# Kernel tuning notes

Measured on AMD Instinct MI355X. Metric: run time of the kernel, lower is better.

Reference implementation:

```python
import jax, jax.numpy as jnp
import numpy as np

N_NODES = 100000
N_EDGES = 800000
N_ETYPES = 5
NUM_GRAPHS = 64
IN_DIM, HID_DIM, OUT_DIM = 23, 128, 64


def setup_inputs() -> dict:
    key = jax.random.key(0)
    ks = jax.random.split(key, 8)
    x = jax.random.normal(ks[0], (N_NODES, IN_DIM), dtype=jnp.float32)
    edges = jax.random.randint(ks[1], (N_ETYPES, 2, N_EDGES), 0, N_NODES, dtype=jnp.int32)
    graph_ids = jnp.sort(jax.random.randint(ks[2], (N_NODES,), 0, NUM_GRAPHS, dtype=jnp.int32))
    # Per-edge-type SAGEConv(gcn) params: fc_neigh weight + bias, two layers.
    W1 = jax.random.normal(ks[3], (N_ETYPES, IN_DIM, HID_DIM), dtype=jnp.float32) / np.sqrt(IN_DIM)
    b1 = jnp.zeros((N_ETYPES, HID_DIM), dtype=jnp.float32)
    W2 = jax.random.normal(ks[4], (N_ETYPES, HID_DIM, OUT_DIM), dtype=jnp.float32) / np.sqrt(HID_DIM)
    b2 = jnp.zeros((N_ETYPES, OUT_DIM), dtype=jnp.float32)
    return {"x": x, "edges": edges, "graph_ids": graph_ids,
            "W1": W1, "b1": b1, "W2": W2, "b2": b2}


def _hetero_sage_gcn(h, edges, W, b):
    """HeteroGraphConv(sum) of SAGEConv(aggregator='gcn') over edge types.
    h: [N, d_in]; edges: [T, 2, E]; W: [T, d_in, d_out]; b: [T, d_out]."""
    n = h.shape[0]

    def per_etype(e, We, be):
        src, dst = e[0], e[1]                                   # [E]
        deg = jax.ops.segment_sum(jnp.ones_like(dst, h.dtype), dst, num_segments=n)
        neigh = jax.ops.segment_sum(h[src], dst, num_segments=n)  # [N, d_in]
        h_neigh = (neigh + h) / (deg[:, None] + 1.0)              # gcn: include self
        return h_neigh @ We + be                                  # fc_neigh only

    outs = jax.vmap(per_etype)(edges, W, b)  # [T, N, d_out]
    return outs.sum(0)


def reference(x, edges, graph_ids, W1, b1, W2, b2):
    h = jax.nn.relu(_hetero_sage_gcn(x, edges, W1, b1))  # dropout = identity (eval)
    h = _hetero_sage_gcn(h, edges, W2, b2)
    counts = jax.ops.segment_sum(jnp.ones(h.shape[0], h.dtype), graph_ids,
                                 num_segments=NUM_GRAPHS)
    pooled = jax.ops.segment_sum(h, graph_ids, num_segments=NUM_GRAPHS)
    return pooled / jnp.maximum(counts, 1.0)[:, None]  # dgl.mean_nodes -> [G, out]
```

## Files before the change

kernel.cpp:

```cpp
#include <hip/hip_runtime.h>

#define N_NODES 100000
#define N_EDGES 800000
#define N_ETYPES 5
#define NUM_GRAPHS 64
#define IN_DIM 23
#define HID_DIM 128
#define OUT_DIM 64
#define N_KEYS (N_NODES * N_ETYPES)
#define KPB 2048
#define NBINS ((N_KEYS + KPB - 1) / KPB)
#define BIN_CAP 18432
#define CHUNK 8192
#define TOT_EDGES (N_EDGES * N_ETYPES)

typedef unsigned short u16;
typedef unsigned int u32;
using short8 = __attribute__((ext_vector_type(8))) short;
using f32x4  = __attribute__((ext_vector_type(4))) float;

__device__ __forceinline__ float bf2f(u16 v) {
    union { unsigned u; float f; } x; x.u = ((unsigned)v) << 16; return x.f;
}
__device__ __forceinline__ float lo2f(u32 v) {
    union { unsigned u; float f; } x; x.u = v << 16; return x.f;
}
__device__ __forceinline__ float hi2f(u32 v) {
    union { unsigned u; float f; } x; x.u = v & 0xffff0000u; return x.f;
}
__device__ __forceinline__ u16 f2bf(float f) {
    union { float f; unsigned u; } x; x.f = f;
    unsigned r = x.u + 0x7fff + ((x.u >> 16) & 1);
    return (u16)(r >> 16);
}

__global__ __launch_bounds__(256) void k_prep(const float* __restrict__ W1,
                                              const float* __restrict__ W2,
                                              const float* __restrict__ b1,
                                              u16* __restrict__ w1t,
                                              u16* __restrict__ w2t,
                                              float* __restrict__ b1s) {
    int stride = gridDim.x * 256;
    int g0 = blockIdx.x * 256 + threadIdx.x;
    for (int i = g0; i < HID_DIM * 160; i += stride) {
        int hid = i / 160, k = i - hid * 160;
        int t = k >> 5, f = k & 31;
        w1t[i] = (f < IN_DIM) ? f2bf(W1[((size_t)t * IN_DIM + f) * HID_DIM + hid]) : (u16)0;
    }
    for (int i = g0; i < N_ETYPES * OUT_DIM * HID_DIM; i += stride) {
        int t = i >> 13, r = i & 8191;
        int out = r >> 7, k = r & 127;
        w2t[i] = f2bf(W2[((size_t)t * HID_DIM + k) * OUT_DIM + out]);
    }
    for (int i = g0; i < HID_DIM; i += stride) {
        float s = 0.f;
        #pragma unroll
        for (int t = 0; t < N_ETYPES; ++t) s += b1[t * HID_DIM + i];
        b1s[i] = s;
    }
}

__global__ __launch_bounds__(256) void k_xb(const float* __restrict__ x,
                                            u16* __restrict__ xb) {
    int i = blockIdx.x * 256 + threadIdx.x;
    if (i >= N_NODES * 32) return;
    int n = i >> 5, f = i & 31;
    xb[i] = (f < IN_DIM) ? f2bf(x[(size_t)n * IN_DIM + f]) : (u16)0;
}

__global__ __launch_bounds__(256) void k_bin(const int* __restrict__ edges,
                                             int* __restrict__ bin_cnt,
                                             int* __restrict__ binned) {
    __shared__ int s_key[CHUNK];
    __shared__ int s_hist[4][256];
    __shared__ int s_base[4][256];
    int tid = threadIdx.x;
    int w = tid >> 6;
    int g0 = blockIdx.x * CHUNK;
    int nch = TOT_EDGES - g0; if (nch > CHUNK) nch = CHUNK;
    for (int i = tid; i < 4 * 256; i += 256) ((int*)s_hist)[i] = 0;
    __syncthreads();
    for (int i = tid; i < nch; i += 256) {
        int gi = g0 + i;
        int t = (unsigned)gi / (unsigned)N_EDGES;
        int e = gi - t * N_EDGES;
        int dst = edges[((size_t)t * 2 + 1) * N_EDGES + e];
        int key = dst * N_ETYPES + t;
        s_key[i] = key;
        atomicAdd(&s_hist[w][key >> 11], 1);
    }
    __syncthreads();
    for (int i = tid; i < NBINS; i += 256) {
        int h0 = s_hist[0][i], h1 = s_hist[1][i], h2 = s_hist[2][i], h3 = s_hist[3][i];
        int h = h0 + h1 + h2 + h3;
        int base = h ? atomicAdd(&bin_cnt[i], h) : 0;
        s_base[0][i] = base;
        s_base[1][i] = base + h0;
        s_base[2][i] = base + h0 + h1;
        s_base[3][i] = base + h0 + h1 + h2;
    }
    __syncthreads();
    for (int i = tid; i < nch; i += 256) {
        int gi = g0 + i;
        int t = (unsigned)gi / (unsigned)N_EDGES;
        int e = gi - t * N_EDGES;
        int src = edges[((size_t)t * 2 + 0) * N_EDGES + e];
        int key = s_key[i];
        int bin = key >> 11;
        int pos = atomicAdd(&s_base[w][bin], 1);
        if (pos < BIN_CAP)
            binned[(size_t)bin * BIN_CAP + pos] = ((key & 2047) << 17) | src;
    }
}

__global__ __launch_bounds__(256) void k_csr(const int* __restrict__ bin_cnt,
                                             const int* __restrict__ binned,
                                             int* __restrict__ rowptr,
                                             int* __restrict__ csr) {
    __shared__ int s_cnt[KPB];
    __shared__ int s_ofs[KPB];
    __shared__ int s_red[256];
    int tid = threadIdx.x;
    int b = blockIdx.x;
    int ps = 0;
    for (int i = tid; i < b; i += 256) ps += bin_cnt[i];
    s_red[tid] = ps;
    __syncthreads();
    for (int s = 128; s > 0; s >>= 1) {
        if (tid < s) s_red[tid] += s_red[tid + s];
        __syncthreads();
    }
    int csr_base = s_red[0];
    __syncthreads();
    int cnt_b = bin_cnt[b];
    if (cnt_b > BIN_CAP) cnt_b = BIN_CAP;
    int key0 = b * KPB;
    int keys_in = N_KEYS - key0; if (keys_in > KPB) keys_in = KPB;
    for (int i = tid; i < KPB; i += 256) s_cnt[i] = 0;
    __syncthreads();
    const int* ep = binned + (size_t)b * BIN_CAP;
    for (int i = tid; i < cnt_b; i += 256)
        atomicAdd(&s_cnt[ep[i] >> 17], 1);
    __syncthreads();
    int loc[8]; int base_t = 0;
    #pragma unroll
    for (int q = 0; q < 8; ++q) { loc[q] = base_t; base_t += s_cnt[tid * 8 + q]; }
    s_red[tid] = base_t;
    __syncthreads();
    for (int s = 1; s < 256; s <<= 1) {
        int add = (tid >= s) ? s_red[tid - s] : 0;
        __syncthreads();
        s_red[tid] += add;
        __syncthreads();
    }
    int excl = (tid == 0) ? 0 : s_red[tid - 1];
    #pragma unroll
    for (int q = 0; q < 8; ++q) {
        int k = tid * 8 + q;
        int o = excl + loc[q];
        s_ofs[k] = o;
        if (k < keys_in) rowptr[key0 + k] = csr_base + o;
    }
    if (b == NBINS - 1 && tid == 0) rowptr[N_KEYS] = csr_base + cnt_b;
    __syncthreads();
    for (int i = tid; i < cnt_b; i += 256) {
        int entry = ep[i];
        int pos = atomicAdd(&s_ofs[entry >> 17], 1);
        csr[csr_base + pos] = entry & 0x1FFFF;
    }
}

__global__ __launch_bounds__(256) void k_gather1(const int* __restrict__ rowptr,
                                                 const int* __restrict__ csr,
                                                 const u32* __restrict__ xb32,
                                                 u32* __restrict__ acat32) {
    int tid = threadIdx.x;
    int lane = tid & 15;
    int lanebase = tid & 48;
    int n = blockIdx.x * 16 + (tid >> 4);
    int t = blockIdx.y;
    int key = n * N_ETYPES + t;
    int rp0 = rowptr[key];
    int deg = rowptr[key + 1] - rp0;
    int stage = csr[rp0 + lane];
    int kmax = deg < 16 ? deg : 16;
    u32 v = xb32[(size_t)n * 16 + lane];
    float acc0 = lo2f(v), acc1 = hi2f(v);
    float a00 = 0.f, a01 = 0.f, a10 = 0.f, a11 = 0.f;
    int k = 0;
    for (; k + 1 < kmax; k += 2) {
        int s0 = __shfl(stage, lanebase + k);
        int s1 = __shfl(stage, lanebase + k + 1);
        u32 v0 = xb32[(size_t)s0 * 16 + lane];
        u32 v1 = xb32[(size_t)s1 * 16 + lane];
        a00 += lo2f(v0); a01 += hi2f(v0);
        a10 += lo2f(v1); a11 += hi2f(v1);
    }
    if (k < kmax) {
        int s0 = __shfl(stage, lanebase + k);
        u32 v0 = xb32[(size_t)s0 * 16 + lane];
        a00 += lo2f(v0); a01 += hi2f(v0);
        ++k;
    }
    for (; k < deg; ++k) {
        int s0 = csr[rp0 + k];
        u32 v0 = xb32[(size_t)s0 * 16 + lane];
        a00 += lo2f(v0); a01 += hi2f(v0);
    }
    acc0 += a00 + a10;
    acc1 += a01 + a11;
    float inv = 1.0f / (float)(deg + 1);
    if (lane < 12)
        acat32[(size_t)n * 60 + t * 12 + lane] =
            (u32)f2bf(acc0 * inv) | ((u32)f2bf(acc1 * inv) << 16);
}

__global__ __launch_bounds__(256) void k_gemm12(const u16* __restrict__ acat,
                                                const u16* __restrict__ w1t,
                                                const u16* __restrict__ w2t,
                                                const float* __restrict__ b1s,
                                                u16* __restrict__ g,
                                                int gt0, int gt1) {
    __shared__ u16 s_a[64 * 168];
    __shared__ u16 s_h1[64 * 136];
    u16* s_out = s_a;
    int tid = threadIdx.x;
    int base = blockIdx.x * 64;

    for (int i = tid; i < 64 * 40; i += 256) {
        int r = i / 40, col4 = i - r * 40;
        int t = col4 >> 3, q4 = col4 & 7;
        ushort4 v = {0, 0, 0, 0};
        if (q4 < 6 && base + r < N_NODES)
            v = *(const ushort4*)&acat[(size_t)(base + r) * 120 + t * 24 + q4 * 4];
        *(ushort4*)&s_a[r * 168 + t * 32 + q4 * 4] = v;
    }
    __syncthreads();

    int l = tid & 63, w = tid >> 6;
    int lr = l & 15, lg = l >> 4;

    short8 a5[5];
    #pragma unroll
    for (int ks = 0; ks < 5; ++ks)
        a5[ks] = *(const short8*)&s_a[(w * 16 + lr) * 168 + ks * 32 + lg * 8];
    {
        f32x4 acc[8];
        #pragma unroll
        for (int nt = 0; nt < 8; ++nt) acc[nt] = (f32x4){0.f, 0.f, 0.f, 0.f};
        #pragma unroll
        for (int nt = 0; nt < 8; ++nt) {
            #pragma unroll
            for (int ks = 0; ks < 5; ++ks) {
                short8 b = *(const short8*)&w1t[(nt * 16 + lr) * 160 + ks * 32 + lg * 8];
                acc[nt] = __builtin_amdgcn_mfma_f32_16x16x32_bf16(a5[ks], b, acc[nt], 0, 0, 0);
            }
        }
        #pragma unroll
        for (int nt = 0; nt < 8; ++nt) {
            float bias = b1s[nt * 16 + lr];
            #pragma unroll
            for (int r = 0; r < 4; ++r) {
                float h = acc[nt][r] + bias;
                s_h1[(w * 16 + lg * 4 + r) * 136 + nt * 16 + lr] = f2bf(h > 0.f ? h : 0.f);
            }
        }
    }
    __syncthreads();

    short8 a2[4];
    #pragma unroll
    for (int ks = 0; ks < 4; ++ks)
        a2[ks] = *(const short8*)&s_h1[(w * 16 + lr) * 136 + ks * 32 + lg * 8];
    for (int t = gt0; t < gt1; ++t) {
        f32x4 acc2[4];
        #pragma unroll
        for (int nt = 0; nt < 4; ++nt) acc2[nt] = (f32x4){0.f, 0.f, 0.f, 0.f};
        #pragma unroll
        for (int nt = 0; nt < 4; ++nt) {
            #pragma unroll
            for (int ks = 0; ks < 4; ++ks) {
                short8 b = *(const short8*)&w2t[((size_t)t * OUT_DIM + nt * 16 + lr) * HID_DIM + ks * 32 + lg * 8];
                acc2[nt] = __builtin_amdgcn_mfma_f32_16x16x32_bf16(a2[ks], b, acc2[nt], 0, 0, 0);
            }
        }
        __syncthreads();
        #pragma unroll
        for (int nt = 0; nt < 4; ++nt)
            #pragma unroll
            for (int r = 0; r < 4; ++r)
                s_out[(w * 16 + lg * 4 + r) * 72 + nt * 16 + lr] = f2bf(acc2[nt][r]);
        __syncthreads();
        size_t pb = (size_t)(t - gt0) * N_NODES;
        #pragma unroll
        for (int j = 0; j < 4; ++j) {
            int flat = j * 256 + tid;
            int rrow = flat >> 4, c4 = (flat & 15) * 4;
            int n = base + rrow;
            if (n < N_NODES)
                *(ushort4*)&g[(pb + n) * OUT_DIM + c4] = *(const ushort4*)&s_out[rrow * 72 + c4];
        }
    }
}

__global__ __launch_bounds__(256) void k_gather2(const int* __restrict__ rowptr,
                                                 const int* __restrict__ csr,
                                                 const u32* __restrict__ g32,
                                                 u32* __restrict__ h232) {
    int tid = threadIdx.x;
    int lane = tid & 31;
    int lanebase = tid & 32;
    int n = blockIdx.x * 8 + (tid >> 5);
    int kb = n * N_ETYPES;
    float acc0 = 0.f, acc1 = 0.f;
    for (int tc = 0; tc < N_ETYPES; ++tc) {
        int rp0 = rowptr[kb + tc];
        int deg = rowptr[kb + tc + 1] - rp0;
        int stage = csr[rp0 + lane];
        int kmax = deg < 32 ? deg : 32;
        const u32* gp = g32 + (size_t)tc * N_NODES * 32;
        u32 v = gp[(size_t)n * 32 + lane];
        float s0 = lo2f(v), s1 = hi2f(v), s2 = 0.f, s3 = 0.f;
        int k = 0;
        for (; k + 1 < kmax; k += 2) {
            int p0 = __shfl(stage, lanebase + k);
            int p1 = __shfl(stage, lanebase + k + 1);
            u32 v0 = gp[(size_t)p0 * 32 + lane];
            u32 v1 = gp[(size_t)p1 * 32 + lane];
            s0 += lo2f(v0); s1 += hi2f(v0);
            s2 += lo2f(v1); s3 += hi2f(v1);
        }
        if (k < kmax) {
            int p0 = __shfl(stage, lanebase + k);
            u32 v0 = gp[(size_t)p0 * 32 + lane];
            s0 += lo2f(v0); s1 += hi2f(v0);
            ++k;
        }
        for (; k < deg; ++k) {
            int p0 = csr[rp0 + k];
            u32 v0 = gp[(size_t)p0 * 32 + lane];
            s0 += lo2f(v0); s1 += hi2f(v0);
        }
        float inv = 1.0f / (float)(deg + 1);
        acc0 += (s0 + s2) * inv;
        acc1 += (s1 + s3) * inv;
    }
    h232[(size_t)n * 32 + lane] = (u32)f2bf(acc0) | ((u32)f2bf(acc1) << 16);
}

__global__ __launch_bounds__(256) void k_pool1(const u16* __restrict__ h2,
                                               const int* __restrict__ gids,
                                               float* __restrict__ out_acc) {
    int w = threadIdx.x >> 6, lane = threadIdx.x & 63;
    int n0 = blockIdx.x * 256 + w * 64;
    int nend = n0 + 64; if (nend > N_NODES) nend = N_NODES;
    float acc = 0.f;
    int cur = -1;
    for (int n = n0; n < nend; ++n) {
        int gid = gids[n];
        if (gid != cur) {
            if (cur >= 0) atomicAdd(&out_acc[cur * OUT_DIM + lane], acc);
            acc = 0.f; cur = gid;
        }
        acc += bf2f(h2[(size_t)n * OUT_DIM + lane]);
    }
    if (cur >= 0) atomicAdd(&out_acc[cur * OUT_DIM + lane], acc);
}

__global__ __launch_bounds__(64) void k_pool2(const float* __restrict__ out_acc,
                                              const int* __restrict__ gids,
                                              const float* __restrict__ b2,
                                              float* __restrict__ out) {
    int gid = blockIdx.x, j = threadIdx.x;
    int lo = 0, hi = N_NODES;
    while (lo < hi) { int mid = (lo + hi) >> 1; if (gids[mid] < gid) lo = mid + 1; else hi = mid; }
    int start = lo;
    hi = N_NODES;
    while (lo < hi) { int mid = (lo + hi) >> 1; if (gids[mid] < gid + 1) lo = mid + 1; else hi = mid; }
    int count = lo - start;
    float b = 0.f;
    #pragma unroll
    for (int t = 0; t < N_ETYPES; ++t) b += b2[t * OUT_DIM + j];
    float c = (float)count;
    out[gid * OUT_DIM + j] = (out_acc[gid * OUT_DIM + j] + c * b) / fmaxf(c, 1.0f);
}

extern "C" void kernel_launch(void* const* d_in, const int* in_sizes, int n_in,
                              void* d_out, int out_size, void* d_ws, size_t ws_size,
                              hipStream_t stream) {
    const float* x    = (const float*)d_in[0];
    const int*   edges= (const int*)d_in[1];
    const int*   gids = (const int*)d_in[2];
    const float* W1   = (const float*)d_in[3];
    const float* b1   = (const float*)d_in[4];
    const float* W2   = (const float*)d_in[5];
    const float* b2   = (const float*)d_in[6];
    float* out = (float*)d_out;

    int*   bin_cnt = (int*)d_ws;
    int*   rowptr  = bin_cnt + 256;
    int*   csr     = bin_cnt + 500272;
    u16*   xb      = (u16*)(bin_cnt + 4500352);
    u16*   w1t     = (u16*)(bin_cnt + 6100352);
    u16*   w2t     = (u16*)(bin_cnt + 6110592);
    float* b1s     = (float*)(bin_cnt + 6131072);
    u16*   acat    = (u16*)(bin_cnt + 6131200);
    u16*   g       = (u16*)(bin_cnt + 12131200);
    int*   binned  = bin_cnt + 12131200;
    u16*   h2      = (u16*)(bin_cnt + 28131200);
    float* out_acc = (float*)(bin_cnt + 31331200);

    hipMemsetAsync(bin_cnt, 0, 256 * sizeof(int), stream);
    hipMemsetAsync(out_acc, 0, NUM_GRAPHS * OUT_DIM * sizeof(float), stream);

    k_prep<<<80, 256, 0, stream>>>(W1, W2, b1, w1t, w2t, b1s);
    k_xb<<<(N_NODES * 32 + 255) / 256, 256, 0, stream>>>(x, xb);
    k_bin<<<(TOT_EDGES + CHUNK - 1) / CHUNK, 256, 0, stream>>>(edges, bin_cnt, binned);
    k_csr<<<NBINS, 256, 0, stream>>>(bin_cnt, binned, rowptr, csr);

    k_gather1<<<dim3(N_NODES / 16, N_ETYPES), 256, 0, stream>>>(
        rowptr, csr, (const u32*)xb, (u32*)acat);

    int nblk = (N_NODES + 63) / 64;
    k_gemm12<<<nblk, 256, 0, stream>>>(acat, w1t, w2t, b1s, g, 0, 5);
    k_gather2<<<N_NODES / 8, 256, 0, stream>>>(rowptr, csr, (const u32*)g, (u32*)h2);

    k_pool1<<<(N_NODES + 255) / 256, 256, 0, stream>>>(h2, gids, out_acc);
    k_pool2<<<NUM_GRAPHS, 64, 0, stream>>>(out_acc, gids, b2, out);
}
```

Measured before the change: 420.6 us.

## Split neighbor gathers across lane groups with shuffle reductions; fuse x conversion into prep

Both gather kernels now give each node a larger lane group split into four sub-groups. Each sub-group walks every fourth neighbor and loads two words per lane, and the partial sums are combined with xor shuffles. This puts more neighbor loads in flight per node to hide latency on the random-access gather, at the cost of more threads per node and extra shuffle reductions. Separately, the bf16 conversion of x is folded into k_prep as a grid-stride loop, removing one kernel launch, and k_prep's grid grows to 1024 blocks.

```diff
diff --git a/kernel.cpp b/kernel.cpp
--- a/kernel.cpp
+++ b/kernel.cpp
@@ -37,9 +37,11 @@
 __global__ __launch_bounds__(256) void k_prep(const float* __restrict__ W1,
                                               const float* __restrict__ W2,
                                               const float* __restrict__ b1,
+                                              const float* __restrict__ x,
                                               u16* __restrict__ w1t,
                                               u16* __restrict__ w2t,
-                                              float* __restrict__ b1s) {
+                                              float* __restrict__ b1s,
+                                              u16* __restrict__ xb) {
     int stride = gridDim.x * 256;
     int g0 = blockIdx.x * 256 + threadIdx.x;
     for (int i = g0; i < HID_DIM * 160; i += stride) {
@@ -58,14 +60,10 @@
         for (int t = 0; t < N_ETYPES; ++t) s += b1[t * HID_DIM + i];
         b1s[i] = s;
     }
-}
-
-__global__ __launch_bounds__(256) void k_xb(const float* __restrict__ x,
-                                            u16* __restrict__ xb) {
-    int i = blockIdx.x * 256 + threadIdx.x;
-    if (i >= N_NODES * 32) return;
-    int n = i >> 5, f = i & 31;
-    xb[i] = (f < IN_DIM) ? f2bf(x[(size_t)n * IN_DIM + f]) : (u16)0;
+    for (int i = g0; i < N_NODES * 32; i += stride) {
+        int n = i >> 5, f = i & 31;
+        xb[i] = (f < IN_DIM) ? f2bf(x[(size_t)n * IN_DIM + f]) : (u16)0;
+    }
 }
 
 __global__ __launch_bounds__(256) void k_bin(const int* __restrict__ edges,
@@ -175,44 +173,68 @@
                                                  const u32* __restrict__ xb32,
                                                  u32* __restrict__ acat32) {
     int tid = threadIdx.x;
-    int lane = tid & 15;
-    int lanebase = tid & 48;
-    int n = blockIdx.x * 16 + (tid >> 4);
+    int lane = tid & 31;
+    int fl = lane & 7;
+    int sub = lane >> 3;
+    int lanebase = tid & 32;
+    int n = blockIdx.x * 8 + (tid >> 5);
     int t = blockIdx.y;
     int key = n * N_ETYPES + t;
     int rp0 = rowptr[key];
     int deg = rowptr[key + 1] - rp0;
     int stage = csr[rp0 + lane];
-    int kmax = deg < 16 ? deg : 16;
-    u32 v = xb32[(size_t)n * 16 + lane];
-    float acc0 = lo2f(v), acc1 = hi2f(v);
-    float a00 = 0.f, a01 = 0.f, a10 = 0.f, a11 = 0.f;
-    int k = 0;
-    for (; k + 1 < kmax; k += 2) {
-        int s0 = __shfl(stage, lanebase + k);
-        int s1 = __shfl(stage, lanebase + k + 1);
-        u32 v0 = xb32[(size_t)s0 * 16 + lane];
-        u32 v1 = xb32[(size_t)s1 * 16 + lane];
-        a00 += lo2f(v0); a01 += hi2f(v0);
-        a10 += lo2f(v1); a11 += hi2f(v1);
-    }
-    if (k < kmax) {
-        int s0 = __shfl(stage, lanebase + k);
-        u32 v0 = xb32[(size_t)s0 * 16 + lane];
-        a00 += lo2f(v0); a01 += hi2f(v0);
-        ++k;
-    }
-    for (; k < deg; ++k) {
-        int s0 = csr[rp0 + k];
-        u32 v0 = xb32[(size_t)s0 * 16 + lane];
-        a00 += lo2f(v0); a01 += hi2f(v0);
-    }
-    acc0 += a00 + a10;
-    acc1 += a01 + a11;
-    float inv = 1.0f / (float)(deg + 1);
-    if (lane < 12)
-        acat32[(size_t)n * 60 + t * 12 + lane] =
-            (u32)f2bf(acc0 * inv) | ((u32)f2bf(acc1 * inv) << 16);
+    int kmax = deg < 32 ? deg : 32;
+    int kend = (kmax + 3) & ~3;
+    float a0 = 0.f, a1 = 0.f, a2 = 0.f, a3 = 0.f;
+    if (sub == 0) {
+        u32 v0 = xb32[(size_t)n * 16 + fl * 2];
+        u32 v1 = xb32[(size_t)n * 16 + fl * 2 + 1];
+        a0 = lo2f(v0); a1 = hi2f(v0); a2 = lo2f(v1); a3 = hi2f(v1);
+    }
+    int k = sub;
+    for (; k + 4 < kend; k += 8) {
+        int sA = __shfl(stage, lanebase + k);
+        int sB = __shfl(stage, lanebase + k + 4);
+        if (k < kmax) {
+            u32 vA0 = xb32[(size_t)sA * 16 + fl * 2];
+            u32 vA1 = xb32[(size_t)sA * 16 + fl * 2 + 1];
+            a0 += lo2f(vA0); a1 += hi2f(vA0);
+            a2 += lo2f(vA1); a3 += hi2f(vA1);
+        }
+        if (k + 4 < kmax) {
+            u32 vB0 = xb32[(size_t)sB * 16 + fl * 2];
+            u32 vB1 = xb32[(size_t)sB * 16 + fl * 2 + 1];
+            a0 += lo2f(vB0); a1 += hi2f(vB0);
+            a2 += lo2f(vB1); a3 += hi2f(vB1);
+        }
+    }
+    if (k < kend) {
+        int sA = __shfl(stage, lanebase + k);
+        if (k < kmax) {
+            u32 vA0 = xb32[(size_t)sA * 16 + fl * 2];
+            u32 vA1 = xb32[(size_t)sA * 16 + fl * 2 + 1];
+            a0 += lo2f(vA0); a1 += hi2f(vA0);
+            a2 += lo2f(vA1); a3 += hi2f(vA1);
+        }
+    }
+    for (int kk = 32 + sub; kk < deg; kk += 4) {
+        int sA = csr[rp0 + kk];
+        u32 vA0 = xb32[(size_t)sA * 16 + fl * 2];
+        u32 vA1 = xb32[(size_t)sA * 16 + fl * 2 + 1];
+        a0 += lo2f(vA0); a1 += hi2f(vA0);
+        a2 += lo2f(vA1); a3 += hi2f(vA1);
+    }
+    a0 += __shfl_xor(a0, 8);  a1 += __shfl_xor(a1, 8);
+    a2 += __shfl_xor(a2, 8);  a3 += __shfl_xor(a3, 8);
+    a0 += __shfl_xor(a0, 16); a1 += __shfl_xor(a1, 16);
+    a2 += __shfl_xor(a2, 16); a3 += __shfl_xor(a3, 16);
+    if (sub == 0 && fl < 6) {
+        float inv = 1.0f / (float)(deg + 1);
+        uint2 o;
+        o.x = (u32)f2bf(a0 * inv) | ((u32)f2bf(a1 * inv) << 16);
+        o.y = (u32)f2bf(a2 * inv) | ((u32)f2bf(a3 * inv) << 16);
+        *(uint2*)&acat32[(size_t)n * 60 + t * 12 + fl * 2] = o;
+    }
 }
 
 __global__ __launch_bounds__(256) void k_gemm12(const u16* __restrict__ acat,
@@ -308,44 +330,72 @@
                                                  const u32* __restrict__ g32,
                                                  u32* __restrict__ h232) {
     int tid = threadIdx.x;
-    int lane = tid & 31;
-    int lanebase = tid & 32;
-    int n = blockIdx.x * 8 + (tid >> 5);
+    int lane = tid & 63;
+    int fl = lane & 15;
+    int sub = lane >> 4;
+    int n = blockIdx.x * 4 + (tid >> 6);
     int kb = n * N_ETYPES;
-    float acc0 = 0.f, acc1 = 0.f;
+    float acc0 = 0.f, acc1 = 0.f, acc2 = 0.f, acc3 = 0.f;
     for (int tc = 0; tc < N_ETYPES; ++tc) {
         int rp0 = rowptr[kb + tc];
         int deg = rowptr[kb + tc + 1] - rp0;
         int stage = csr[rp0 + lane];
-        int kmax = deg < 32 ? deg : 32;
+        int kmax = deg < 64 ? deg : 64;
+        int kend = (kmax + 3) & ~3;
         const u32* gp = g32 + (size_t)tc * N_NODES * 32;
-        u32 v = gp[(size_t)n * 32 + lane];
-        float s0 = lo2f(v), s1 = hi2f(v), s2 = 0.f, s3 = 0.f;
-        int k = 0;
-        for (; k + 1 < kmax; k += 2) {
-            int p0 = __shfl(stage, lanebase + k);
-            int p1 = __shfl(stage, lanebase + k + 1);
-            u32 v0 = gp[(size_t)p0 * 32 + lane];
-            u32 v1 = gp[(size_t)p1 * 32 + lane];
-            s0 += lo2f(v0); s1 += hi2f(v0);
-            s2 += lo2f(v1); s3 += hi2f(v1);
-        }
-        if (k < kmax) {
-            int p0 = __shfl(stage, lanebase + k);
-            u32 v0 = gp[(size_t)p0 * 32 + lane];
-            s0 += lo2f(v0); s1 += hi2f(v0);
-            ++k;
-        }
-        for (; k < deg; ++k) {
-            int p0 = csr[rp0 + k];
-            u32 v0 = gp[(size_t)p0 * 32 + lane];
-            s0 += lo2f(v0); s1 += hi2f(v0);
+        float s0 = 0.f, s1 = 0.f, s2 = 0.f, s3 = 0.f;
+        if (sub == 0) {
+            u32 v0 = gp[(size_t)n * 32 + fl * 2];
+            u32 v1 = gp[(size_t)n * 32 + fl * 2 + 1];
+            s0 = lo2f(v0); s1 = hi2f(v0); s2 = lo2f(v1); s3 = hi2f(v1);
+        }
+        int k = sub;
+        for (; k + 4 < kend; k += 8) {
+            int pA = __shfl(stage, k);
+            int pB = __shfl(stage, k + 4);
+            if (k < kmax) {
+                u32 vA0 = gp[(size_t)pA * 32 + fl * 2];
+                u32 vA1 = gp[(size_t)pA * 32 + fl * 2 + 1];
+                s0 += lo2f(vA0); s1 += hi2f(vA0);
+                s2 += lo2f(vA1); s3 += hi2f(vA1);
+            }
+            if (k + 4 < kmax) {
+                u32 vB0 = gp[(size_t)pB * 32 + fl * 2];
+                u32 vB1 = gp[(size_t)pB * 32 + fl * 2 + 1];
+                s0 += lo2f(vB0); s1 += hi2f(vB0);
+                s2 += lo2f(vB1); s3 += hi2f(vB1);
+            }
+        }
+        if (k < kend) {
+            int pA = __shfl(stage, k);
+            if (k < kmax) {
+                u32 vA0 = gp[(size_t)pA * 32 + fl * 2];
+                u32 vA1 = gp[(size_t)pA * 32 + fl * 2 + 1];
+                s0 += lo2f(vA0); s1 += hi2f(vA0);
+                s2 += lo2f(vA1); s3 += hi2f(vA1);
+            }
+        }
+        for (int kk = 64 + sub; kk < deg; kk += 4) {
+            int pA = csr[rp0 + kk];
+            u32 vA0 = gp[(size_t)pA * 32 + fl * 2];
+            u32 vA1 = gp[(size_t)pA * 32 + fl * 2 + 1];
+            s0 += lo2f(vA0); s1 += hi2f(vA0);
+            s2 += lo2f(vA1); s3 += hi2f(vA1);
         }
         float inv = 1.0f / (float)(deg + 1);
-        acc0 += (s0 + s2) * inv;
-        acc1 += (s1 + s3) * inv;
-    }
-    h232[(size_t)n * 32 + lane] = (u32)f2bf(acc0) | ((u32)f2bf(acc1) << 16);
+        acc0 += s0 * inv; acc1 += s1 * inv;
+        acc2 += s2 * inv; acc3 += s3 * inv;
+    }
+    acc0 += __shfl_xor(acc0, 16); acc1 += __shfl_xor(acc1, 16);
+    acc2 += __shfl_xor(acc2, 16); acc3 += __shfl_xor(acc3, 16);
+    acc0 += __shfl_xor(acc0, 32); acc1 += __shfl_xor(acc1, 32);
+    acc2 += __shfl_xor(acc2, 32); acc3 += __shfl_xor(acc3, 32);
+    if (sub == 0) {
+        uint2 o;
+        o.x = (u32)f2bf(acc0) | ((u32)f2bf(acc1) << 16);
+        o.y = (u32)f2bf(acc2) | ((u32)f2bf(acc3) << 16);
+        *(uint2*)&h232[(size_t)n * 32 + fl * 2] = o;
+    }
 }
 
 __global__ __launch_bounds__(256) void k_pool1(const u16* __restrict__ h2,
@@ -413,17 +463,16 @@
     hipMemsetAsync(bin_cnt, 0, 256 * sizeof(int), stream);
     hipMemsetAsync(out_acc, 0, NUM_GRAPHS * OUT_DIM * sizeof(float), stream);
 
-    k_prep<<<80, 256, 0, stream>>>(W1, W2, b1, w1t, w2t, b1s);
-    k_xb<<<(N_NODES * 32 + 255) / 256, 256, 0, stream>>>(x, xb);
+    k_prep<<<1024, 256, 0, stream>>>(W1, W2, b1, x, w1t, w2t, b1s, xb);
     k_bin<<<(TOT_EDGES + CHUNK - 1) / CHUNK, 256, 0, stream>>>(edges, bin_cnt, binned);
     k_csr<<<NBINS, 256, 0, stream>>>(bin_cnt, binned, rowptr, csr);
 
-    k_gather1<<<dim3(N_NODES / 16, N_ETYPES), 256, 0, stream>>>(
+    k_gather1<<<dim3(N_NODES / 8, N_ETYPES), 256, 0, stream>>>(
         rowptr, csr, (const u32*)xb, (u32*)acat);
 
     int nblk = (N_NODES + 63) / 64;
     k_gemm12<<<nblk, 256, 0, stream>>>(acat, w1t, w2t, b1s, g, 0, 5);
-    k_gather2<<<N_NODES / 8, 256, 0, stream>>>(rowptr, csr, (const u32*)g, (u32*)h2);
+    k_gather2<<<N_NODES / 4, 256, 0, stream>>>(rowptr, csr, (const u32*)g, (u32*)h2);
 
     k_pool1<<<(N_NODES + 255) / 256, 256, 0, stream>>>(h2, gids, out_acc);
     k_pool2<<<NUM_GRAPHS, 64, 0, stream>>>(out_acc, gids, b2, out);
```

After: 452.0 us. 1.07x slower.

## Fuse prep kernels into binning launch and widen gather loads to 8 bytes

Applied to the files above, without the earlier changes.

Folds the weight/bias prep and x-to-bf16 conversion into extra blocks of the binning kernel, removing two launches and letting that conversion run alongside binning. Both gather kernels now use half as many lanes per node, each loading uint2 (four bf16 values) per neighbor, with 4-way unrolled neighbor loops and the index stage split across two registers. This is meant to raise bytes per memory request and memory-level parallelism in the latency-bound gathers. In exchange it adds register pressure, and the k_bin prep blocks now have to cover the whole of xb with only 64 blocks.

```diff
diff --git a/kernel.cpp b/kernel.cpp
--- a/kernel.cpp
+++ b/kernel.cpp
@@ -13,6 +13,8 @@
 #define BIN_CAP 18432
 #define CHUNK 8192
 #define TOT_EDGES (N_EDGES * N_ETYPES)
+#define BIN_BLOCKS ((TOT_EDGES + CHUNK - 1) / CHUNK)
+#define PREP_BLOCKS 64
 
 typedef unsigned short u16;
 typedef unsigned int u32;
@@ -34,47 +36,48 @@
     return (u16)(r >> 16);
 }
 
-__global__ __launch_bounds__(256) void k_prep(const float* __restrict__ W1,
-                                              const float* __restrict__ W2,
-                                              const float* __restrict__ b1,
-                                              u16* __restrict__ w1t,
-                                              u16* __restrict__ w2t,
-                                              float* __restrict__ b1s) {
-    int stride = gridDim.x * 256;
-    int g0 = blockIdx.x * 256 + threadIdx.x;
-    for (int i = g0; i < HID_DIM * 160; i += stride) {
-        int hid = i / 160, k = i - hid * 160;
-        int t = k >> 5, f = k & 31;
-        w1t[i] = (f < IN_DIM) ? f2bf(W1[((size_t)t * IN_DIM + f) * HID_DIM + hid]) : (u16)0;
-    }
-    for (int i = g0; i < N_ETYPES * OUT_DIM * HID_DIM; i += stride) {
-        int t = i >> 13, r = i & 8191;
-        int out = r >> 7, k = r & 127;
-        w2t[i] = f2bf(W2[((size_t)t * HID_DIM + k) * OUT_DIM + out]);
-    }
-    for (int i = g0; i < HID_DIM; i += stride) {
-        float s = 0.f;
-        #pragma unroll
-        for (int t = 0; t < N_ETYPES; ++t) s += b1[t * HID_DIM + i];
-        b1s[i] = s;
-    }
-}
-
-__global__ __launch_bounds__(256) void k_xb(const float* __restrict__ x,
-                                            u16* __restrict__ xb) {
-    int i = blockIdx.x * 256 + threadIdx.x;
-    if (i >= N_NODES * 32) return;
-    int n = i >> 5, f = i & 31;
-    xb[i] = (f < IN_DIM) ? f2bf(x[(size_t)n * IN_DIM + f]) : (u16)0;
-}
-
 __global__ __launch_bounds__(256) void k_bin(const int* __restrict__ edges,
                                              int* __restrict__ bin_cnt,
-                                             int* __restrict__ binned) {
+                                             int* __restrict__ binned,
+                                             const float* __restrict__ W1,
+                                             const float* __restrict__ W2,
+                                             const float* __restrict__ b1,
+                                             const float* __restrict__ x,
+                                             u16* __restrict__ w1t,
+                                             u16* __restrict__ w2t,
+                                             float* __restrict__ b1s,
+                                             u16* __restrict__ xb) {
     __shared__ int s_key[CHUNK];
     __shared__ int s_hist[4][256];
     __shared__ int s_base[4][256];
     int tid = threadIdx.x;
+
+    if (blockIdx.x >= BIN_BLOCKS) {
+        int stride = PREP_BLOCKS * 256;
+        int g0 = (blockIdx.x - BIN_BLOCKS) * 256 + tid;
+        for (int i = g0; i < HID_DIM * 160; i += stride) {
+            int hid = i / 160, k = i - hid * 160;
+            int t = k >> 5, f = k & 31;
+            w1t[i] = (f < IN_DIM) ? f2bf(W1[((size_t)t * IN_DIM + f) * HID_DIM + hid]) : (u16)0;
+        }
+        for (int i = g0; i < N_ETYPES * OUT_DIM * HID_DIM; i += stride) {
+            int t = i >> 13, r = i & 8191;
+            int out = r >> 7, k = r & 127;
+            w2t[i] = f2bf(W2[((size_t)t * HID_DIM + k) * OUT_DIM + out]);
+        }
+        for (int i = g0; i < HID_DIM; i += stride) {
+            float s = 0.f;
+            #pragma unroll
+            for (int t = 0; t < N_ETYPES; ++t) s += b1[t * HID_DIM + i];
+            b1s[i] = s;
+        }
+        for (int i = g0; i < N_NODES * 32; i += stride) {
+            int n = i >> 5, f = i & 31;
+            xb[i] = (f < IN_DIM) ? f2bf(x[(size_t)n * IN_DIM + f]) : (u16)0;
+        }
+        return;
+    }
+
     int w = tid >> 6;
     int g0 = blockIdx.x * CHUNK;
     int nch = TOT_EDGES - g0; if (nch > CHUNK) nch = CHUNK;
@@ -175,44 +178,72 @@
                                                  const u32* __restrict__ xb32,
                                                  u32* __restrict__ acat32) {
     int tid = threadIdx.x;
-    int lane = tid & 15;
-    int lanebase = tid & 48;
-    int n = blockIdx.x * 16 + (tid >> 4);
+    int fl = tid & 7;
+    int lanebase = tid & 56;
+    int n = blockIdx.x * 32 + (tid >> 3);
     int t = blockIdx.y;
     int key = n * N_ETYPES + t;
     int rp0 = rowptr[key];
     int deg = rowptr[key + 1] - rp0;
-    int stage = csr[rp0 + lane];
+    int stageA = csr[rp0 + fl];
+    int stageB = csr[rp0 + 8 + fl];
     int kmax = deg < 16 ? deg : 16;
-    u32 v = xb32[(size_t)n * 16 + lane];
-    float acc0 = lo2f(v), acc1 = hi2f(v);
-    float a00 = 0.f, a01 = 0.f, a10 = 0.f, a11 = 0.f;
+    int kA = kmax < 8 ? kmax : 8;
+    uint2 v = *(const uint2*)&xb32[(size_t)n * 16 + fl * 2];
+    float a0 = lo2f(v.x), a1 = hi2f(v.x), a2 = lo2f(v.y), a3 = hi2f(v.y);
+    float b0 = 0.f, b1v = 0.f, b2 = 0.f, b3 = 0.f;
     int k = 0;
-    for (; k + 1 < kmax; k += 2) {
-        int s0 = __shfl(stage, lanebase + k);
-        int s1 = __shfl(stage, lanebase + k + 1);
-        u32 v0 = xb32[(size_t)s0 * 16 + lane];
-        u32 v1 = xb32[(size_t)s1 * 16 + lane];
-        a00 += lo2f(v0); a01 += hi2f(v0);
-        a10 += lo2f(v1); a11 += hi2f(v1);
-    }
-    if (k < kmax) {
-        int s0 = __shfl(stage, lanebase + k);
-        u32 v0 = xb32[(size_t)s0 * 16 + lane];
-        a00 += lo2f(v0); a01 += hi2f(v0);
-        ++k;
-    }
-    for (; k < deg; ++k) {
+    for (; k + 3 < kA; k += 4) {
+        int s0 = __shfl(stageA, lanebase + k);
+        int s1 = __shfl(stageA, lanebase + k + 1);
+        int s2 = __shfl(stageA, lanebase + k + 2);
+        int s3 = __shfl(stageA, lanebase + k + 3);
+        uint2 v0 = *(const uint2*)&xb32[(size_t)s0 * 16 + fl * 2];
+        uint2 v1 = *(const uint2*)&xb32[(size_t)s1 * 16 + fl * 2];
+        uint2 v2 = *(const uint2*)&xb32[(size_t)s2 * 16 + fl * 2];
+        uint2 v3 = *(const uint2*)&xb32[(size_t)s3 * 16 + fl * 2];
+        a0 += lo2f(v0.x); a1 += hi2f(v0.x); a2 += lo2f(v0.y); a3 += hi2f(v0.y);
+        b0 += lo2f(v1.x); b1v += hi2f(v1.x); b2 += lo2f(v1.y); b3 += hi2f(v1.y);
+        a0 += lo2f(v2.x); a1 += hi2f(v2.x); a2 += lo2f(v2.y); a3 += hi2f(v2.y);
+        b0 += lo2f(v3.x); b1v += hi2f(v3.x); b2 += lo2f(v3.y); b3 += hi2f(v3.y);
+    }
+    for (; k < kA; ++k) {
+        int s0 = __shfl(stageA, lanebase + k);
+        uint2 v0 = *(const uint2*)&xb32[(size_t)s0 * 16 + fl * 2];
+        a0 += lo2f(v0.x); a1 += hi2f(v0.x); a2 += lo2f(v0.y); a3 += hi2f(v0.y);
+    }
+    for (k = 8; k + 3 < kmax; k += 4) {
+        int s0 = __shfl(stageB, lanebase + k - 8);
+        int s1 = __shfl(stageB, lanebase + k - 7);
+        int s2 = __shfl(stageB, lanebase + k - 6);
+        int s3 = __shfl(stageB, lanebase + k - 5);
+        uint2 v0 = *(const uint2*)&xb32[(size_t)s0 * 16 + fl * 2];
+        uint2 v1 = *(const uint2*)&xb32[(size_t)s1 * 16 + fl * 2];
+        uint2 v2 = *(const uint2*)&xb32[(size_t)s2 * 16 + fl * 2];
+        uint2 v3 = *(const uint2*)&xb32[(size_t)s3 * 16 + fl * 2];
+        a0 += lo2f(v0.x); a1 += hi2f(v0.x); a2 += lo2f(v0.y); a3 += hi2f(v0.y);
+        b0 += lo2f(v1.x); b1v += hi2f(v1.x); b2 += lo2f(v1.y); b3 += hi2f(v1.y);
+        a0 += lo2f(v2.x); a1 += hi2f(v2.x); a2 += lo2f(v2.y); a3 += hi2f(v2.y);
+        b0 += lo2f(v3.x); b1v += hi2f(v3.x); b2 += lo2f(v3.y); b3 += hi2f(v3.y);
+    }
+    for (; k < kmax && k >= 8; ++k) {
+        int s0 = __shfl(stageB, lanebase + k - 8);
+        uint2 v0 = *(const uint2*)&xb32[(size_t)s0 * 16 + fl * 2];
+        a0 += lo2f(v0.x); a1 += hi2f(v0.x); a2 += lo2f(v0.y); a3 += hi2f(v0.y);
+    }
+    for (k = 16; k < deg; ++k) {
         int s0 = csr[rp0 + k];
-        u32 v0 = xb32[(size_t)s0 * 16 + lane];
-        a00 += lo2f(v0); a01 += hi2f(v0);
-    }
-    acc0 += a00 + a10;
-    acc1 += a01 + a11;
-    float inv = 1.0f / (float)(deg + 1);
-    if (lane < 12)
-        acat32[(size_t)n * 60 + t * 12 + lane] =
-            (u32)f2bf(acc0 * inv) | ((u32)f2bf(acc1 * inv) << 16);
+        uint2 v0 = *(const uint2*)&xb32[(size_t)s0 * 16 + fl * 2];
+        a0 += lo2f(v0.x); a1 += hi2f(v0.x); a2 += lo2f(v0.y); a3 += hi2f(v0.y);
+    }
+    a0 += b0; a1 += b1v; a2 += b2; a3 += b3;
+    if (fl < 6) {
+        float inv = 1.0f / (float)(deg + 1);
+        uint2 o;
+        o.x = (u32)f2bf(a0 * inv) | ((u32)f2bf(a1 * inv) << 16);
+        o.y = (u32)f2bf(a2 * inv) | ((u32)f2bf(a3 * inv) << 16);
+        *(uint2*)&acat32[(size_t)n * 60 + t * 12 + fl * 2] = o;
+    }
 }
 
 __global__ __launch_bounds__(256) void k_gemm12(const u16* __restrict__ acat,
@@ -308,44 +339,76 @@
                                                  const u32* __restrict__ g32,
                                                  u32* __restrict__ h232) {
     int tid = threadIdx.x;
-    int lane = tid & 31;
-    int lanebase = tid & 32;
-    int n = blockIdx.x * 8 + (tid >> 5);
+    int fl = tid & 15;
+    int lanebase = tid & 48;
+    int n = blockIdx.x * 16 + (tid >> 4);
     int kb = n * N_ETYPES;
-    float acc0 = 0.f, acc1 = 0.f;
+    float acc0 = 0.f, acc1 = 0.f, acc2 = 0.f, acc3 = 0.f;
     for (int tc = 0; tc < N_ETYPES; ++tc) {
         int rp0 = rowptr[kb + tc];
         int deg = rowptr[kb + tc + 1] - rp0;
-        int stage = csr[rp0 + lane];
+        int stageA = csr[rp0 + fl];
+        int stageB = csr[rp0 + 16 + fl];
         int kmax = deg < 32 ? deg : 32;
+        int kA = kmax < 16 ? kmax : 16;
         const u32* gp = g32 + (size_t)tc * N_NODES * 32;
-        u32 v = gp[(size_t)n * 32 + lane];
-        float s0 = lo2f(v), s1 = hi2f(v), s2 = 0.f, s3 = 0.f;
+        uint2 v = *(const uint2*)&gp[(size_t)n * 32 + fl * 2];
+        float s0 = lo2f(v.x), s1 = hi2f(v.x), s2 = lo2f(v.y), s3 = hi2f(v.y);
+        float r0 = 0.f, r1 = 0.f, r2 = 0.f, r3 = 0.f;
         int k = 0;
-        for (; k + 1 < kmax; k += 2) {
-            int p0 = __shfl(stage, lanebase + k);
-            int p1 = __shfl(stage, lanebase + k + 1);
-            u32 v0 = gp[(size_t)p0 * 32 + lane];
-            u32 v1 = gp[(size_t)p1 * 32 + lane];
-            s0 += lo2f(v0); s1 += hi2f(v0);
-            s2 += lo2f(v1); s3 += hi2f(v1);
-        }
-        if (k < kmax) {
-            int p0 = __shfl(stage, lanebase + k);
-            u32 v0 = gp[(size_t)p0 * 32 + lane];
-            s0 += lo2f(v0); s1 += hi2f(v0);
-            ++k;
-        }
-        for (; k < deg; ++k) {
+        for (; k + 3 < kA; k += 4) {
+            int p0 = __shfl(stageA, lanebase + k);
+            int p1 = __shfl(stageA, lanebase + k + 1);
+            int p2 = __shfl(stageA, lanebase + k + 2);
+            int p3 = __shfl(stageA, lanebase + k + 3);
+            uint2 v0 = *(const uint2*)&gp[(size_t)p0 * 32 + fl * 2];
+            uint2 v1 = *(const uint2*)&gp[(size_t)p1 * 32 + fl * 2];
+            uint2 v2 = *(const uint2*)&gp[(size_t)p2 * 32 + fl * 2];
+            uint2 v3 = *(const uint2*)&gp[(size_t)p3 * 32 + fl * 2];
+            s0 += lo2f(v0.x); s1 += hi2f(v0.x); s2 += lo2f(v0.y); s3 += hi2f(v0.y);
+            r0 += lo2f(v1.x); r1 += hi2f(v1.x); r2 += lo2f(v1.y); r3 += hi2f(v1.y);
+            s0 += lo2f(v2.x); s1 += hi2f(v2.x); s2 += lo2f(v2.y); s3 += hi2f(v2.y);
+            r0 += lo2f(v3.x); r1 += hi2f(v3.x); r2 += lo2f(v3.y); r3 += hi2f(v3.y);
+        }
+        for (; k < kA; ++k) {
+            int p0 = __shfl(stageA, lanebase + k);
+            uint2 v0 = *(const uint2*)&gp[(size_t)p0 * 32 + fl * 2];
+            s0 += lo2f(v0.x); s1 += hi2f(v0.x); s2 += lo2f(v0.y); s3 += hi2f(v0.y);
+        }
+        for (k = 16; k + 3 < kmax; k += 4) {
+            int p0 = __shfl(stageB, lanebase + k - 16);
+            int p1 = __shfl(stageB, lanebase + k - 15);
+            int p2 = __shfl(stageB, lanebase + k - 14);
+            int p3 = __shfl(stageB, lanebase + k - 13);
+            uint2 v0 = *(const uint2*)&gp[(size_t)p0 * 32 + fl * 2];
+            uint2 v1 = *(const uint2*)&gp[(size_t)p1 * 32 + fl * 2];
+            uint2 v2 = *(const uint2*)&gp[(size_t)p2 * 32 + fl * 2];
+            uint2 v3 = *(const uint2*)&gp[(size_t)p3 * 32 + fl * 2];
+            s0 += lo2f(v0.x); s1 += hi2f(v0.x); s2 += lo2f(v0.y); s3 += hi2f(v0.y);
+            r0 += lo2f(v1.x); r1 += hi2f(v1.x); r2 += lo2f(v1.y); r3 += hi2f(v1.y);
+            s0 += lo2f(v2.x); s1 += hi2f(v2.x); s2 += lo2f(v2.y); s3 += hi2f(v2.y);
+            r0 += lo2f(v3.x); r1 += hi2f(v3.x); r2 += lo2f(v3.y); r3 += hi2f(v3.y);
+        }
+        for (; k < kmax && k >= 16; ++k) {
+            int p0 = __shfl(stageB, lanebase + k - 16);
+            uint2 v0 = *(const uint2*)&gp[(size_t)p0 * 32 + fl * 2];
+            s0 += lo2f(v0.x); s1 += hi2f(v0.x); s2 += lo2f(v0.y); s3 += hi2f(v0.y);
+        }
+        for (k = 32; k < deg; ++k) {
             int p0 = csr[rp0 + k];
-            u32 v0 = gp[(size_t)p0 * 32 + lane];
-            s0 += lo2f(v0); s1 += hi2f(v0);
+            uint2 v0 = *(const uint2*)&gp[(size_t)p0 * 32 + fl * 2];
+            s0 += lo2f(v0.x); s1 += hi2f(v0.x); s2 += lo2f(v0.y); s3 += hi2f(v0.y);
         }
         float inv = 1.0f / (float)(deg + 1);
-        acc0 += (s0 + s2) * inv;
-        acc1 += (s1 + s3) * inv;
-    }
-    h232[(size_t)n * 32 + lane] = (u32)f2bf(acc0) | ((u32)f2bf(acc1) << 16);
+        acc0 = fmaf(s0 + r0, inv, acc0);
+        acc1 = fmaf(s1 + r1, inv, acc1);
+        acc2 = fmaf(s2 + r2, inv, acc2);
+        acc3 = fmaf(s3 + r3, inv, acc3);
+    }
+    uint2 o;
+    o.x = (u32)f2bf(acc0) | ((u32)f2bf(acc1) << 16);
+    o.y = (u32)f2bf(acc2) | ((u32)f2bf(acc3) << 16);
+    *(uint2*)&h232[(size_t)n * 32 + fl * 2] = o;
 }
 
 __global__ __launch_bounds__(256) void k_pool1(const u16* __restrict__ h2,
@@ -413,17 +476,16 @@
     hipMemsetAsync(bin_cnt, 0, 256 * sizeof(int), stream);
     hipMemsetAsync(out_acc, 0, NUM_GRAPHS * OUT_DIM * sizeof(float), stream);
 
-    k_prep<<<80, 256, 0, stream>>>(W1, W2, b1, w1t, w2t, b1s);
-    k_xb<<<(N_NODES * 32 + 255) / 256, 256, 0, stream>>>(x, xb);
-    k_bin<<<(TOT_EDGES + CHUNK - 1) / CHUNK, 256, 0, stream>>>(edges, bin_cnt, binned);
+    k_bin<<<BIN_BLOCKS + PREP_BLOCKS, 256, 0, stream>>>(
+        edges, bin_cnt, binned, W1, W2, b1, x, w1t, w2t, b1s, xb);
     k_csr<<<NBINS, 256, 0, stream>>>(bin_cnt, binned, rowptr, csr);
 
-    k_gather1<<<dim3(N_NODES / 16, N_ETYPES), 256, 0, stream>>>(
+    k_gather1<<<dim3(N_NODES / 32, N_ETYPES), 256, 0, stream>>>(
         rowptr, csr, (const u32*)xb, (u32*)acat);
 
     int nblk = (N_NODES + 63) / 64;
     k_gemm12<<<nblk, 256, 0, stream>>>(acat, w1t, w2t, b1s, g, 0, 5);
-    k_gather2<<<N_NODES / 8, 256, 0, stream>>>(rowptr, csr, (const u32*)g, (u32*)h2);
+    k_gather2<<<N_NODES / 16, 256, 0, stream>>>(rowptr, csr, (const u32*)g, (u32*)h2);
 
     k_pool1<<<(N_NODES + 255) / 256, 256, 0, stream>>>(h2, gids, out_acc);
     k_pool2<<<NUM_GRAPHS, 64, 0, stream>>>(out_acc, gids, b2, out);
```

Measured after the change: 429.7 us. 1.02x slower.
